# Performance work log

Hardware: AMD Instinct MI355X
Metric: run time of the kernel (lower is better)

## Reference

```python
import jax, jax.numpy as jnp
import numpy as np

N_NODES = 50000
N_EDGES = 800000
N_FEAT = 128
D_HID = 128
N_CLASS = 40


def gcn_conv(x, W, b, src, dst, n_nodes):
    """PyG GCNConv: h = D^{-1/2} (A + I) D^{-1/2} (x @ W) + b.
    src/dst are int arrays [E]; self-loops handled analytically."""
    h = x @ W  # [N, D]
    ones = jnp.ones(src.shape[0], dtype=h.dtype)
    # degree after adding self-loops: 1 + in-degree (edge weights are 1)
    deg = 1.0 + jax.ops.segment_sum(ones, dst, num_segments=n_nodes)
    dinv = jax.lax.rsqrt(deg)  # [N]
    # messages along edges src -> dst with symmetric normalization
    msg = h[src] * (dinv[src] * dinv[dst])[:, None]  # [E, D]
    agg = jax.ops.segment_sum(msg, dst, num_segments=n_nodes)  # [N, D]
    # self-loop contribution: dinv[i]^2 * h[i]
    agg = agg + h * (dinv * dinv)[:, None]
    return agg + b


def setup_inputs() -> dict:
    key = jax.random.key(0)
    ks = jax.random.split(key, 5)
    x = jax.random.normal(ks[0], (N_NODES, N_FEAT), dtype=jnp.float32)
    edge_index = jax.random.randint(ks[1], (2, N_EDGES), 0, N_NODES, dtype=jnp.int64)
    s_in = 1.0 / np.sqrt(N_FEAT)
    s_h = 1.0 / np.sqrt(D_HID)
    W_in = jax.random.normal(ks[2], (N_FEAT, D_HID), dtype=jnp.float32) * s_in
    W1 = jax.random.normal(ks[3], (D_HID, D_HID), dtype=jnp.float32) * s_h
    W_out = jax.random.normal(ks[4], (D_HID, N_CLASS), dtype=jnp.float32) * s_h
    return {
        "x": x,
        "edge_index": edge_index,
        "W_in": W_in,
        "b_in": jnp.zeros((D_HID,), jnp.float32),
        "W1": W1,
        "b1": jnp.zeros((D_HID,), jnp.float32),
        "W_out": W_out,
        "b_out": jnp.zeros((N_CLASS,), jnp.float32),
    }


def reference(x, edge_index, W_in, b_in, W1, b1, W_out, b_out):
    src, dst = edge_index[0], edge_index[1]
    n = x.shape[0]
    # input GCNConv (no activation on input_fc, matching the torch forward)
    h = gcn_conv(x, W_in, b_in, src, dst, n)
    # hidden layer: dropout is identity at eval; relu after conv; normalize=False
    h = jax.nn.relu(gcn_conv(h, W1, b1, src, dst, n))
    out = h @ W_out + b_out
    return jax.nn.log_softmax(out, axis=1)
```

## Files before the change

kernel.cpp:

```cpp
#include <hip/hip_runtime.h>
#include <math.h>


#define THREADS 256

typedef __attribute__((ext_vector_type(8))) short short8v;
typedef __attribute__((ext_vector_type(4))) float float4v;

__device__ __forceinline__ float b2f(unsigned int lo16) {
    return __uint_as_float(lo16 << 16);
}
__device__ __forceinline__ unsigned short f2b(float f) {
    unsigned int u = __float_as_uint(f);
    u += 0x7FFFu + ((u >> 16) & 1u);
    return (unsigned short)(u >> 16);
}

__global__ void detect_idx64(const int* __restrict__ idx, int* __restrict__ flag) {
    int t = threadIdx.x;
    unsigned long long b = __ballot(idx[2 * t + 1] == 0);
    if (t == 0) *flag = (b == 0xFFFFFFFFFFFFFFFFull) ? 1 : 0;
}

__global__ void fill_pos(const int* __restrict__ idx, const int* __restrict__ flag,
                         int* __restrict__ cnt, unsigned int* __restrict__ rec, int E) {
    int e = blockIdx.x * blockDim.x + threadIdx.x;
    if (e >= E) return;
    int f = *flag;
    int src, dst;
    if (f) { src = idx[2 * e]; dst = idx[2 * (E + e)]; }
    else   { src = idx[e];     dst = idx[E + e]; }
    unsigned int pos = (unsigned int)atomicAdd(&cnt[dst], 1);
    rec[e] = ((unsigned int)src << 16) | (pos & 0xFFFFu);
}

__global__ __launch_bounds__(256) void scanA(const int* __restrict__ cnt,
                                             int* __restrict__ bsum, int N) {
    __shared__ int wt[4];
    int tid = threadIdx.x, lane = tid & 63, w = tid >> 6;
    int i = blockIdx.x * 256 + tid;
    int v = (i < N) ? cnt[i] : 0;
    int s = v;
#pragma unroll
    for (int off = 1; off < 64; off <<= 1) {
        int t = __shfl_up(s, off);
        if (lane >= off) s += t;
    }
    if (lane == 63) wt[w] = s;
    __syncthreads();
    if (tid == 0) bsum[blockIdx.x] = wt[0] + wt[1] + wt[2] + wt[3];
}

__global__ __launch_bounds__(256) void scanB(int* __restrict__ bsum,
                                             int* __restrict__ boff,
                                             int* __restrict__ rowstart,
                                             int nb, int N) {
    __shared__ int wt[4];
    __shared__ int wo[5];
    int tid = threadIdx.x, lane = tid & 63, w = tid >> 6;
    int v = (tid < nb) ? bsum[tid] : 0;
    int s = v;
#pragma unroll
    for (int off = 1; off < 64; off <<= 1) {
        int t = __shfl_up(s, off);
        if (lane >= off) s += t;
    }
    if (lane == 63) wt[w] = s;
    __syncthreads();
    if (tid == 0) {
        int run = 0;
#pragma unroll
        for (int k = 0; k < 4; ++k) { wo[k] = run; run += wt[k]; }
        wo[4] = run;
    }
    __syncthreads();
    if (tid < nb) boff[tid] = wo[w] + s - v;
    if (tid == 0) rowstart[N] = wo[4];
}

__global__ __launch_bounds__(256) void scanC(const int* __restrict__ cnt,
                                             const int* __restrict__ boff,
                                             int* __restrict__ rowstart,
                                             float* __restrict__ dinv, int N) {
    __shared__ int wt[4];
    __shared__ int wo[4];
    int tid = threadIdx.x, lane = tid & 63, w = tid >> 6;
    int i = blockIdx.x * 256 + tid;
    int v = (i < N) ? cnt[i] : 0;
    int s = v;
#pragma unroll
    for (int off = 1; off < 64; off <<= 1) {
        int t = __shfl_up(s, off);
        if (lane >= off) s += t;
    }
    if (lane == 63) wt[w] = s;
    __syncthreads();
    if (tid == 0) {
        int run = 0;
#pragma unroll
        for (int k = 0; k < 4; ++k) { wo[k] = run; run += wt[k]; }
    }
    __syncthreads();
    if (i < N) {
        rowstart[i] = boff[blockIdx.x] + wo[w] + (s - v);
        dinv[i] = rsqrtf(1.0f + (float)v);
    }
}

__global__ void fill_place(const int* __restrict__ idx, const int* __restrict__ flag,
                           const unsigned int* __restrict__ rec,
                           const int* __restrict__ rowstart,
                           unsigned short* __restrict__ srcs, int E) {
    int e = blockIdx.x * blockDim.x + threadIdx.x;
    if (e >= E) return;
    int f = *flag;
    int dst = f ? idx[2 * (E + e)] : idx[E + e];
    unsigned int r = rec[e];
    srcs[rowstart[dst] + (int)(r & 0xFFFFu)] = (unsigned short)(r >> 16);
}

__global__ __launch_bounds__(256) void pack_w2(const float* __restrict__ W0,
                                               const float* __restrict__ W1,
                                               uint4* __restrict__ wpk0,
                                               uint4* __restrict__ wpk1) {
    const float* W = blockIdx.x ? W1 : W0;
    uint4* wpk = blockIdx.x ? wpk1 : wpk0;
    int tid = threadIdx.x;
    for (int it = 0; it < 8; ++it) {
        int s = it * 256 + tid;
        int ct = s >> 8;
        int kb = (s >> 6) & 3;
        int l  = s & 63;
        int col = ct * 16 + (l & 15);
        int k0  = kb * 32 + ((l >> 4) << 3);
        unsigned short e0 = f2b(W[(k0 + 0) * 128 + col]);
        unsigned short e1 = f2b(W[(k0 + 1) * 128 + col]);
        unsigned short e2 = f2b(W[(k0 + 2) * 128 + col]);
        unsigned short e3 = f2b(W[(k0 + 3) * 128 + col]);
        unsigned short e4 = f2b(W[(k0 + 4) * 128 + col]);
        unsigned short e5 = f2b(W[(k0 + 5) * 128 + col]);
        unsigned short e6 = f2b(W[(k0 + 6) * 128 + col]);
        unsigned short e7 = f2b(W[(k0 + 7) * 128 + col]);
        uint4 u;
        u.x = (unsigned int)e0 | ((unsigned int)e1 << 16);
        u.y = (unsigned int)e2 | ((unsigned int)e3 << 16);
        u.z = (unsigned int)e4 | ((unsigned int)e5 << 16);
        u.w = (unsigned int)e6 | ((unsigned int)e7 << 16);
        wpk[s] = u;
    }
}

template <int ABF>
__global__ __launch_bounds__(256) void gemm_mfma(const void* __restrict__ Ap,
                                                 const uint4* __restrict__ wpk,
                                                 unsigned short* __restrict__ outb,
                                                 int N) {
    __shared__ unsigned short ol[128 * 128];
    int tid = threadIdx.x;
    int w = tid >> 6, l = tid & 63;
    int lr = l & 15, lq = l >> 4;
    int base = blockIdx.x * 128;
    int arow0 = base + w * 16 + lr;
    int arow1 = base + 64 + w * 16 + lr;
    int ar0 = (arow0 < N) ? arow0 : (N - 1);
    int ar1 = (arow1 < N) ? arow1 : (N - 1);

    float4v acc[2][8];
#pragma unroll
    for (int t = 0; t < 2; ++t)
#pragma unroll
        for (int ct = 0; ct < 8; ++ct) acc[t][ct] = (float4v){0.f, 0.f, 0.f, 0.f};

#pragma unroll
    for (int kb = 0; kb < 4; ++kb) {
        short8v af0, af1;
        if (ABF) {
            uint4 v0 = *(const uint4*)((const unsigned short*)Ap + (size_t)ar0 * 128 + kb * 32 + lq * 8);
            uint4 v1 = *(const uint4*)((const unsigned short*)Ap + (size_t)ar1 * 128 + kb * 32 + lq * 8);
            union { uint4 u; short8v s; } c0, c1; c0.u = v0; c1.u = v1;
            af0 = c0.s; af1 = c1.s;
        } else {
            const float* a0 = (const float*)Ap + (size_t)ar0 * 128 + kb * 32 + lq * 8;
            const float* a1 = (const float*)Ap + (size_t)ar1 * 128 + kb * 32 + lq * 8;
            float4 va0 = *(const float4*)a0, vb0 = *(const float4*)(a0 + 4);
            float4 va1 = *(const float4*)a1, vb1 = *(const float4*)(a1 + 4);
            uint4 u0, u1;
            u0.x = (unsigned int)f2b(va0.x) | ((unsigned int)f2b(va0.y) << 16);
            u0.y = (unsigned int)f2b(va0.z) | ((unsigned int)f2b(va0.w) << 16);
            u0.z = (unsigned int)f2b(vb0.x) | ((unsigned int)f2b(vb0.y) << 16);
            u0.w = (unsigned int)f2b(vb0.z) | ((unsigned int)f2b(vb0.w) << 16);
            u1.x = (unsigned int)f2b(va1.x) | ((unsigned int)f2b(va1.y) << 16);
            u1.y = (unsigned int)f2b(va1.z) | ((unsigned int)f2b(va1.w) << 16);
            u1.z = (unsigned int)f2b(vb1.x) | ((unsigned int)f2b(vb1.y) << 16);
            u1.w = (unsigned int)f2b(vb1.z) | ((unsigned int)f2b(vb1.w) << 16);
            union { uint4 uu; short8v s; } c0, c1; c0.uu = u0; c1.uu = u1;
            af0 = c0.s; af1 = c1.s;
        }
#pragma unroll
        for (int ct = 0; ct < 8; ++ct) {
            uint4 bv = wpk[(ct * 4 + kb) * 64 + l];
            union { uint4 u; short8v s; } cv; cv.u = bv; short8v bf = cv.s;
            acc[0][ct] = __builtin_amdgcn_mfma_f32_16x16x32_bf16(af0, bf, acc[0][ct], 0, 0, 0);
            acc[1][ct] = __builtin_amdgcn_mfma_f32_16x16x32_bf16(af1, bf, acc[1][ct], 0, 0, 0);
        }
    }

#pragma unroll
    for (int t = 0; t < 2; ++t)
#pragma unroll
        for (int ct = 0; ct < 8; ++ct)
#pragma unroll
            for (int r = 0; r < 4; ++r)
                ol[(t * 64 + w * 16 + lq * 4 + r) * 128 + ct * 16 + lr] = f2b(acc[t][ct][r]);
    __syncthreads();
#pragma unroll
    for (int it = 0; it < 8; ++it) {
        int o = it * 4096 + tid * 16;
        int rr = o >> 8;
        int cb = o & 255;
        int gr = base + rr;
        if (gr < N) {
            uint4 v = *(const uint4*)((const char*)ol + o);
            *(uint4*)((char*)outb + (size_t)gr * 256 + cb) = v;
        }
    }
}

__global__ __launch_bounds__(256) void agg_node(const unsigned short* __restrict__ hb,
                                                const int* __restrict__ rowstart,
                                                const unsigned short* __restrict__ srcs,
                                                const float* __restrict__ dinv,
                                                const float* __restrict__ b,
                                                unsigned short* __restrict__ outb,
                                                int N, int do_relu) {
    int w = threadIdx.x >> 6, lane = threadIdx.x & 63;
    int node = blockIdx.x * 4 + w;
    if (node >= N) return;
    int beg = rowstart[node], end = rowstart[node + 1];
    float dn = dinv[node];
    int quarter = lane >> 4, q = lane & 15;
    const uint4* hb8 = (const uint4*)hb;
    float a0 = 0.f, a1 = 0.f, a2 = 0.f, a3 = 0.f;
    float a4 = 0.f, a5 = 0.f, a6 = 0.f, a7 = 0.f;

    for (int j0 = beg; j0 < end; j0 += 64) {
        int myj = j0 + lane;
        int ms = 0;
        float md = 0.f;
        if (myj < end) { ms = (int)srcs[myj]; md = dinv[ms]; }
        int m = min(64, end - j0);
#pragma unroll 2
        for (int k = 0; k < m; k += 8) {
            int i0 = k + quarter;
            int i1 = k + 4 + quarter;
            int s0 = __shfl(ms, i0);
            int s1 = __shfl(ms, i1);
            float c0 = dn * __shfl(md, i0);
            float c1 = dn * __shfl(md, i1);
            uint4 v0 = hb8[(size_t)s0 * 16 + q];
            uint4 v1 = hb8[(size_t)s1 * 16 + q];
            a0 += c0 * b2f(v0.x & 0xFFFFu);
            a1 += c0 * b2f(v0.x >> 16);
            a2 += c0 * b2f(v0.y & 0xFFFFu);
            a3 += c0 * b2f(v0.y >> 16);
            a4 += c0 * b2f(v0.z & 0xFFFFu);
            a5 += c0 * b2f(v0.z >> 16);
            a6 += c0 * b2f(v0.w & 0xFFFFu);
            a7 += c0 * b2f(v0.w >> 16);
            a0 += c1 * b2f(v1.x & 0xFFFFu);
            a1 += c1 * b2f(v1.x >> 16);
            a2 += c1 * b2f(v1.y & 0xFFFFu);
            a3 += c1 * b2f(v1.y >> 16);
            a4 += c1 * b2f(v1.z & 0xFFFFu);
            a5 += c1 * b2f(v1.z >> 16);
            a6 += c1 * b2f(v1.w & 0xFFFFu);
            a7 += c1 * b2f(v1.w >> 16);
        }
    }
    a0 += __shfl_xor(a0, 32); a1 += __shfl_xor(a1, 32);
    a2 += __shfl_xor(a2, 32); a3 += __shfl_xor(a3, 32);
    a4 += __shfl_xor(a4, 32); a5 += __shfl_xor(a5, 32);
    a6 += __shfl_xor(a6, 32); a7 += __shfl_xor(a7, 32);
    a0 += __shfl_xor(a0, 16); a1 += __shfl_xor(a1, 16);
    a2 += __shfl_xor(a2, 16); a3 += __shfl_xor(a3, 16);
    a4 += __shfl_xor(a4, 16); a5 += __shfl_xor(a5, 16);
    a6 += __shfl_xor(a6, 16); a7 += __shfl_xor(a7, 16);

    if (quarter == 0) {
        uint4 sv = hb8[(size_t)node * 16 + q];
        float d2 = dn * dn;
        float4 b0 = ((const float4*)b)[2 * q];
        float4 b1 = ((const float4*)b)[2 * q + 1];
        float r0 = a0 + d2 * b2f(sv.x & 0xFFFFu) + b0.x;
        float r1 = a1 + d2 * b2f(sv.x >> 16)     + b0.y;
        float r2 = a2 + d2 * b2f(sv.y & 0xFFFFu) + b0.z;
        float r3 = a3 + d2 * b2f(sv.y >> 16)     + b0.w;
        float r4 = a4 + d2 * b2f(sv.z & 0xFFFFu) + b1.x;
        float r5 = a5 + d2 * b2f(sv.z >> 16)     + b1.y;
        float r6 = a6 + d2 * b2f(sv.w & 0xFFFFu) + b1.z;
        float r7 = a7 + d2 * b2f(sv.w >> 16)     + b1.w;
        if (do_relu) {
            r0 = fmaxf(r0, 0.f); r1 = fmaxf(r1, 0.f);
            r2 = fmaxf(r2, 0.f); r3 = fmaxf(r3, 0.f);
            r4 = fmaxf(r4, 0.f); r5 = fmaxf(r5, 0.f);
            r6 = fmaxf(r6, 0.f); r7 = fmaxf(r7, 0.f);
        }
        uint4 o;
        o.x = (unsigned int)f2b(r0) | ((unsigned int)f2b(r1) << 16);
        o.y = (unsigned int)f2b(r2) | ((unsigned int)f2b(r3) << 16);
        o.z = (unsigned int)f2b(r4) | ((unsigned int)f2b(r5) << 16);
        o.w = (unsigned int)f2b(r6) | ((unsigned int)f2b(r7) << 16);
        ((uint4*)outb)[(size_t)node * 16 + q] = o;
    }
}

__global__ __launch_bounds__(256) void out_gemm(const unsigned short* __restrict__ h2b,
                                                const float* __restrict__ Wout,
                                                const float* __restrict__ bout,
                                                float* __restrict__ out, int N) {
    __shared__ float Xt[128 * 128];
    __shared__ float Wl[128 * 40];
    __shared__ float bl[40];
    int tid = threadIdx.x;
    int row0 = blockIdx.x * 128;

    for (int i = tid; i < 128 * 40; i += 256) Wl[i] = Wout[i];
    if (tid < 40) bl[tid] = bout[tid];

    {
        int r = tid >> 1, kh = tid & 1;
        int gr = row0 + r;
#pragma unroll
        for (int i = 0; i < 16; ++i) {
            int k = kh * 64 + i * 4;
            float f0, f1, f2, f3;
            if (gr < N) {
                uint2 qv = ((const uint2*)h2b)[(size_t)gr * 32 + (k >> 2)];
                f0 = b2f(qv.x & 0xFFFFu); f1 = b2f(qv.x >> 16);
                f2 = b2f(qv.y & 0xFFFFu); f3 = b2f(qv.y >> 16);
            } else {
                f0 = f1 = f2 = f3 = 0.f;
            }
            Xt[(k + 0) * 128 + r] = f0;
            Xt[(k + 1) * 128 + r] = f1;
            Xt[(k + 2) * 128 + r] = f2;
            Xt[(k + 3) * 128 + r] = f3;
        }
    }
    __syncthreads();

    int cg = tid & 7;
    int r4 = tid >> 3;
    float bias[5];
#pragma unroll
    for (int c = 0; c < 5; ++c) bias[c] = bl[5 * cg + c];

    float acc[4][5];
#pragma unroll
    for (int j = 0; j < 4; ++j)
#pragma unroll
        for (int c = 0; c < 5; ++c) acc[j][c] = 0.f;

    const float4* Xt4 = (const float4*)Xt;
#pragma unroll 4
    for (int k = 0; k < 128; ++k) {
        float4 xv = Xt4[k * 32 + r4];
        const float* wr = &Wl[k * 40 + 5 * cg];
        float w0 = wr[0], w1 = wr[1], w2 = wr[2], w3 = wr[3], w4 = wr[4];
        float xs[4] = {xv.x, xv.y, xv.z, xv.w};
#pragma unroll
        for (int j = 0; j < 4; ++j) {
            acc[j][0] += xs[j] * w0;
            acc[j][1] += xs[j] * w1;
            acc[j][2] += xs[j] * w2;
            acc[j][3] += xs[j] * w3;
            acc[j][4] += xs[j] * w4;
        }
    }

#pragma unroll
    for (int j = 0; j < 4; ++j) {
        int r = row0 + r4 * 4 + j;
        if (r >= N) continue;
        float v[5];
        float m = -INFINITY;
#pragma unroll
        for (int c = 0; c < 5; ++c) { v[c] = acc[j][c] + bias[c]; m = fmaxf(m, v[c]); }
        m = fmaxf(m, __shfl_xor(m, 1));
        m = fmaxf(m, __shfl_xor(m, 2));
        m = fmaxf(m, __shfl_xor(m, 4));
        float s = 0.f;
#pragma unroll
        for (int c = 0; c < 5; ++c) s += expf(v[c] - m);
        s += __shfl_xor(s, 1);
        s += __shfl_xor(s, 2);
        s += __shfl_xor(s, 4);
        float ls = logf(s);
#pragma unroll
        for (int c = 0; c < 5; ++c) out[(size_t)r * 40 + 5 * cg + c] = v[c] - m - ls;
    }
}

static inline size_t al256(size_t x) { return (x + 255) & ~(size_t)255; }

extern "C" void kernel_launch(void* const* d_in, const int* in_sizes, int n_in,
                              void* d_out, int out_size, void* d_ws, size_t ws_size,
                              hipStream_t stream) {
    const float* x     = (const float*)d_in[0];
    const int*   idx   = (const int*)d_in[1];
    const float* W_in  = (const float*)d_in[2];
    const float* b_in  = (const float*)d_in[3];
    const float* W1    = (const float*)d_in[4];
    const float* b1    = (const float*)d_in[5];
    const float* W_out = (const float*)d_in[6];
    const float* b_out = (const float*)d_in[7];
    float* out = (float*)d_out;

    int N = in_sizes[0] / 128;
    int E = in_sizes[1] / 2;

    char* ws = (char*)d_ws;
    size_t off = 0;
    int* flag = (int*)(ws + off);              off += 256;
    int* cnt = (int*)(ws + off);               off += al256((size_t)N * 4);
    int* rowstart = (int*)(ws + off);          off += al256((size_t)(N + 1) * 4);
    float* dinv = (float*)(ws + off);          off += al256((size_t)N * 4);
    unsigned short* srcs = (unsigned short*)(ws + off); off += al256((size_t)E * 2);
    unsigned int* rec = (unsigned int*)(ws + off);      off += al256((size_t)E * 4);
    int* bsum = (int*)(ws + off);              off += 2048;
    int* boff = (int*)(ws + off);              off += 2048;
    uint4* wpk1 = (uint4*)(ws + off);          off += 32768;
    uint4* wpk2 = (uint4*)(ws + off);          off += 32768;
    unsigned short* B0 = (unsigned short*)(ws + off);   off += (size_t)N * 128 * 2;
    unsigned short* B1 = (unsigned short*)(ws + off);

    int nb_e = (E + THREADS - 1) / THREADS;
    int nb_n = (N + THREADS - 1) / THREADS;
    int nb_g = (N + 127) / 128;
    int nb_a = (N + 3) / 4;

    detect_idx64<<<1, 64, 0, stream>>>(idx, flag);
    hipMemsetAsync(cnt, 0, (size_t)N * 4, stream);
    pack_w2<<<2, THREADS, 0, stream>>>(W_in, W1, wpk1, wpk2);
    fill_pos<<<nb_e, THREADS, 0, stream>>>(idx, flag, cnt, rec, E);
    scanA<<<nb_n, THREADS, 0, stream>>>(cnt, bsum, N);
    scanB<<<1, THREADS, 0, stream>>>(bsum, boff, rowstart, nb_n, N);
    scanC<<<nb_n, THREADS, 0, stream>>>(cnt, boff, rowstart, dinv, N);
    fill_place<<<nb_e, THREADS, 0, stream>>>(idx, flag, rec, rowstart, srcs, E);

    gemm_mfma<0><<<nb_g, THREADS, 0, stream>>>(x, wpk1, B0, N);
    agg_node<<<nb_a, THREADS, 0, stream>>>(B0, rowstart, srcs, dinv, b_in,
                                           B1, N, 0);
    gemm_mfma<1><<<nb_g, THREADS, 0, stream>>>(B1, wpk2, B0, N);
    agg_node<<<nb_a, THREADS, 0, stream>>>(B0, rowstart, srcs, dinv, b1,
                                           B1, N, 1);
    out_gemm<<<nb_g, THREADS, 0, stream>>>(B1, W_out, b_out, out, N);
}
```

Before: 260.6 us.

## Merge setup kernels and co-schedule first GEMM with edge counting

Replaces the flag-detect kernel, the count memset and the weight packing with one init kernel that also pre-converts x to bf16. The first-layer GEMM then runs in the same launch as the edge-position atomic pass, with separate blocks for each, so the two independent jobs overlap and fewer kernels are launched. The cost is an extra pass that writes and re-reads a bf16 copy of x. The agg loop also loses its unroll-2 pragma, which may change how well its loads are scheduled.

```diff
diff --git a/kernel.cpp b/kernel.cpp
--- a/kernel.cpp
+++ b/kernel.cpp
@@ -16,15 +16,116 @@
     return (unsigned short)(u >> 16);
 }
 
-__global__ void detect_idx64(const int* __restrict__ idx, int* __restrict__ flag) {
-    int t = threadIdx.x;
-    unsigned long long b = __ballot(idx[2 * t + 1] == 0);
-    if (t == 0) *flag = (b == 0xFFFFFFFFFFFFFFFFull) ? 1 : 0;
-}
-
-__global__ void fill_pos(const int* __restrict__ idx, const int* __restrict__ flag,
-                         int* __restrict__ cnt, unsigned int* __restrict__ rec, int E) {
-    int e = blockIdx.x * blockDim.x + threadIdx.x;
+__global__ __launch_bounds__(256) void f_init(const float* __restrict__ x,
+                                              const int* __restrict__ idx,
+                                              const float* __restrict__ W0,
+                                              const float* __restrict__ W1f,
+                                              int* __restrict__ flag,
+                                              int* __restrict__ cnt,
+                                              uint4* __restrict__ wpk0,
+                                              uint4* __restrict__ wpk1,
+                                              unsigned short* __restrict__ Xb,
+                                              int N) {
+    int tid = threadIdx.x, bid = blockIdx.x, nb = gridDim.x;
+    if (bid == 0 && tid < 64) {
+        unsigned long long b = __ballot(idx[2 * tid + 1] == 0);
+        if (tid == 0) *flag = (b == 0xFFFFFFFFFFFFFFFFull) ? 1 : 0;
+    }
+    for (int i = bid * 256 + tid; i < N; i += nb * 256) cnt[i] = 0;
+    if (bid < 2) {
+        const float* W = bid ? W1f : W0;
+        uint4* wpk = bid ? wpk1 : wpk0;
+#pragma unroll
+        for (int it = 0; it < 8; ++it) {
+            int s = it * 256 + tid;
+            int ct = s >> 8, kb = (s >> 6) & 3, l = s & 63;
+            int col = ct * 16 + (l & 15);
+            int k0 = kb * 32 + ((l >> 4) << 3);
+            uint4 u;
+            u.x = (unsigned int)f2b(W[(k0 + 0) * 128 + col]) | ((unsigned int)f2b(W[(k0 + 1) * 128 + col]) << 16);
+            u.y = (unsigned int)f2b(W[(k0 + 2) * 128 + col]) | ((unsigned int)f2b(W[(k0 + 3) * 128 + col]) << 16);
+            u.z = (unsigned int)f2b(W[(k0 + 4) * 128 + col]) | ((unsigned int)f2b(W[(k0 + 5) * 128 + col]) << 16);
+            u.w = (unsigned int)f2b(W[(k0 + 6) * 128 + col]) | ((unsigned int)f2b(W[(k0 + 7) * 128 + col]) << 16);
+            wpk[s] = u;
+        }
+    }
+    int total = N * 32;
+    const float4* x4 = (const float4*)x;
+    ushort4* xb4 = (ushort4*)Xb;
+    for (int i = bid * 256 + tid; i < total; i += nb * 256) {
+        float4 v = x4[i];
+        ushort4 o;
+        o.x = f2b(v.x); o.y = f2b(v.y); o.z = f2b(v.z); o.w = f2b(v.w);
+        xb4[i] = o;
+    }
+}
+
+__device__ __forceinline__ void gemm_body(const unsigned short* __restrict__ Ab,
+                                          const uint4* __restrict__ wpk,
+                                          unsigned short* __restrict__ outb,
+                                          unsigned short* ol, int base, int N) {
+    int tid = threadIdx.x;
+    int w = tid >> 6, l = tid & 63;
+    int lr = l & 15, lq = l >> 4;
+    int arow0 = base + w * 16 + lr;
+    int arow1 = base + 64 + w * 16 + lr;
+    int ar0 = (arow0 < N) ? arow0 : (N - 1);
+    int ar1 = (arow1 < N) ? arow1 : (N - 1);
+
+    float4v acc[2][8];
+#pragma unroll
+    for (int t = 0; t < 2; ++t)
+#pragma unroll
+        for (int ct = 0; ct < 8; ++ct) acc[t][ct] = (float4v){0.f, 0.f, 0.f, 0.f};
+
+#pragma unroll
+    for (int kb = 0; kb < 4; ++kb) {
+        uint4 v0 = *(const uint4*)(Ab + (size_t)ar0 * 128 + kb * 32 + lq * 8);
+        uint4 v1 = *(const uint4*)(Ab + (size_t)ar1 * 128 + kb * 32 + lq * 8);
+        union { uint4 u; short8v s; } c0, c1; c0.u = v0; c1.u = v1;
+        short8v af0 = c0.s, af1 = c1.s;
+#pragma unroll
+        for (int ct = 0; ct < 8; ++ct) {
+            uint4 bv = wpk[(ct * 4 + kb) * 64 + l];
+            union { uint4 u; short8v s; } cv; cv.u = bv; short8v bf = cv.s;
+            acc[0][ct] = __builtin_amdgcn_mfma_f32_16x16x32_bf16(af0, bf, acc[0][ct], 0, 0, 0);
+            acc[1][ct] = __builtin_amdgcn_mfma_f32_16x16x32_bf16(af1, bf, acc[1][ct], 0, 0, 0);
+        }
+    }
+#pragma unroll
+    for (int t = 0; t < 2; ++t)
+#pragma unroll
+        for (int ct = 0; ct < 8; ++ct)
+#pragma unroll
+            for (int r = 0; r < 4; ++r)
+                ol[(t * 64 + w * 16 + lq * 4 + r) * 128 + ct * 16 + lr] = f2b(acc[t][ct][r]);
+    __syncthreads();
+#pragma unroll
+    for (int it = 0; it < 8; ++it) {
+        int o = it * 4096 + tid * 16;
+        int rr = o >> 8, cb = o & 255;
+        int gr = base + rr;
+        if (gr < N) {
+            uint4 v = *(const uint4*)((const char*)ol + o);
+            *(uint4*)((char*)outb + (size_t)gr * 256 + cb) = v;
+        }
+    }
+}
+
+__global__ __launch_bounds__(256) void f_g1fp(const unsigned short* __restrict__ Xb,
+                                              const uint4* __restrict__ wpk1,
+                                              unsigned short* __restrict__ B0,
+                                              const int* __restrict__ idx,
+                                              const int* __restrict__ flag,
+                                              int* __restrict__ cnt,
+                                              unsigned int* __restrict__ rec,
+                                              int N, int E, int nbg) {
+    __shared__ unsigned short ol[128 * 128];
+    if ((int)blockIdx.x < nbg) {
+        gemm_body(Xb, wpk1, B0, ol, blockIdx.x * 128, N);
+        return;
+    }
+    int e = (blockIdx.x - nbg) * 256 + threadIdx.x;
     if (e >= E) return;
     int f = *flag;
     int src, dst;
@@ -32,6 +133,14 @@
     else   { src = idx[e];     dst = idx[E + e]; }
     unsigned int pos = (unsigned int)atomicAdd(&cnt[dst], 1);
     rec[e] = ((unsigned int)src << 16) | (pos & 0xFFFFu);
+}
+
+__global__ __launch_bounds__(256) void gemm_mfma(const unsigned short* __restrict__ Ab,
+                                                 const uint4* __restrict__ wpk,
+                                                 unsigned short* __restrict__ outb,
+                                                 int N) {
+    __shared__ unsigned short ol[128 * 128];
+    gemm_body(Ab, wpk, outb, ol, blockIdx.x * 128, N);
 }
 
 __global__ __launch_bounds__(256) void scanA(const int* __restrict__ cnt,
@@ -117,113 +226,6 @@
     int dst = f ? idx[2 * (E + e)] : idx[E + e];
     unsigned int r = rec[e];
     srcs[rowstart[dst] + (int)(r & 0xFFFFu)] = (unsigned short)(r >> 16);
-}
-
-__global__ __launch_bounds__(256) void pack_w2(const float* __restrict__ W0,
-                                               const float* __restrict__ W1,
-                                               uint4* __restrict__ wpk0,
-                                               uint4* __restrict__ wpk1) {
-    const float* W = blockIdx.x ? W1 : W0;
-    uint4* wpk = blockIdx.x ? wpk1 : wpk0;
-    int tid = threadIdx.x;
-    for (int it = 0; it < 8; ++it) {
-        int s = it * 256 + tid;
-        int ct = s >> 8;
-        int kb = (s >> 6) & 3;
-        int l  = s & 63;
-        int col = ct * 16 + (l & 15);
-        int k0  = kb * 32 + ((l >> 4) << 3);
-        unsigned short e0 = f2b(W[(k0 + 0) * 128 + col]);
-        unsigned short e1 = f2b(W[(k0 + 1) * 128 + col]);
-        unsigned short e2 = f2b(W[(k0 + 2) * 128 + col]);
-        unsigned short e3 = f2b(W[(k0 + 3) * 128 + col]);
-        unsigned short e4 = f2b(W[(k0 + 4) * 128 + col]);
-        unsigned short e5 = f2b(W[(k0 + 5) * 128 + col]);
-        unsigned short e6 = f2b(W[(k0 + 6) * 128 + col]);
-        unsigned short e7 = f2b(W[(k0 + 7) * 128 + col]);
-        uint4 u;
-        u.x = (unsigned int)e0 | ((unsigned int)e1 << 16);
-        u.y = (unsigned int)e2 | ((unsigned int)e3 << 16);
-        u.z = (unsigned int)e4 | ((unsigned int)e5 << 16);
-        u.w = (unsigned int)e6 | ((unsigned int)e7 << 16);
-        wpk[s] = u;
-    }
-}
-
-template <int ABF>
-__global__ __launch_bounds__(256) void gemm_mfma(const void* __restrict__ Ap,
-                                                 const uint4* __restrict__ wpk,
-                                                 unsigned short* __restrict__ outb,
-                                                 int N) {
-    __shared__ unsigned short ol[128 * 128];
-    int tid = threadIdx.x;
-    int w = tid >> 6, l = tid & 63;
-    int lr = l & 15, lq = l >> 4;
-    int base = blockIdx.x * 128;
-    int arow0 = base + w * 16 + lr;
-    int arow1 = base + 64 + w * 16 + lr;
-    int ar0 = (arow0 < N) ? arow0 : (N - 1);
-    int ar1 = (arow1 < N) ? arow1 : (N - 1);
-
-    float4v acc[2][8];
-#pragma unroll
-    for (int t = 0; t < 2; ++t)
-#pragma unroll
-        for (int ct = 0; ct < 8; ++ct) acc[t][ct] = (float4v){0.f, 0.f, 0.f, 0.f};
-
-#pragma unroll
-    for (int kb = 0; kb < 4; ++kb) {
-        short8v af0, af1;
-        if (ABF) {
-            uint4 v0 = *(const uint4*)((const unsigned short*)Ap + (size_t)ar0 * 128 + kb * 32 + lq * 8);
-            uint4 v1 = *(const uint4*)((const unsigned short*)Ap + (size_t)ar1 * 128 + kb * 32 + lq * 8);
-            union { uint4 u; short8v s; } c0, c1; c0.u = v0; c1.u = v1;
-            af0 = c0.s; af1 = c1.s;
-        } else {
-            const float* a0 = (const float*)Ap + (size_t)ar0 * 128 + kb * 32 + lq * 8;
-            const float* a1 = (const float*)Ap + (size_t)ar1 * 128 + kb * 32 + lq * 8;
-            float4 va0 = *(const float4*)a0, vb0 = *(const float4*)(a0 + 4);
-            float4 va1 = *(const float4*)a1, vb1 = *(const float4*)(a1 + 4);
-            uint4 u0, u1;
-            u0.x = (unsigned int)f2b(va0.x) | ((unsigned int)f2b(va0.y) << 16);
-            u0.y = (unsigned int)f2b(va0.z) | ((unsigned int)f2b(va0.w) << 16);
-            u0.z = (unsigned int)f2b(vb0.x) | ((unsigned int)f2b(vb0.y) << 16);
-            u0.w = (unsigned int)f2b(vb0.z) | ((unsigned int)f2b(vb0.w) << 16);
-            u1.x = (unsigned int)f2b(va1.x) | ((unsigned int)f2b(va1.y) << 16);
-            u1.y = (unsigned int)f2b(va1.z) | ((unsigned int)f2b(va1.w) << 16);
-            u1.z = (unsigned int)f2b(vb1.x) | ((unsigned int)f2b(vb1.y) << 16);
-            u1.w = (unsigned int)f2b(vb1.z) | ((unsigned int)f2b(vb1.w) << 16);
-            union { uint4 uu; short8v s; } c0, c1; c0.uu = u0; c1.uu = u1;
-            af0 = c0.s; af1 = c1.s;
-        }
-#pragma unroll
-        for (int ct = 0; ct < 8; ++ct) {
-            uint4 bv = wpk[(ct * 4 + kb) * 64 + l];
-            union { uint4 u; short8v s; } cv; cv.u = bv; short8v bf = cv.s;
-            acc[0][ct] = __builtin_amdgcn_mfma_f32_16x16x32_bf16(af0, bf, acc[0][ct], 0, 0, 0);
-            acc[1][ct] = __builtin_amdgcn_mfma_f32_16x16x32_bf16(af1, bf, acc[1][ct], 0, 0, 0);
-        }
-    }
-
-#pragma unroll
-    for (int t = 0; t < 2; ++t)
-#pragma unroll
-        for (int ct = 0; ct < 8; ++ct)
-#pragma unroll
-            for (int r = 0; r < 4; ++r)
-                ol[(t * 64 + w * 16 + lq * 4 + r) * 128 + ct * 16 + lr] = f2b(acc[t][ct][r]);
-    __syncthreads();
-#pragma unroll
-    for (int it = 0; it < 8; ++it) {
-        int o = it * 4096 + tid * 16;
-        int rr = o >> 8;
-        int cb = o & 255;
-        int gr = base + rr;
-        if (gr < N) {
-            uint4 v = *(const uint4*)((const char*)ol + o);
-            *(uint4*)((char*)outb + (size_t)gr * 256 + cb) = v;
-        }
-    }
 }
 
 __global__ __launch_bounds__(256) void agg_node(const unsigned short* __restrict__ hb,
@@ -245,11 +247,9 @@
 
     for (int j0 = beg; j0 < end; j0 += 64) {
         int myj = j0 + lane;
-        int ms = 0;
-        float md = 0.f;
+        int ms = 0; float md = 0.f;
         if (myj < end) { ms = (int)srcs[myj]; md = dinv[ms]; }
         int m = min(64, end - j0);
-#pragma unroll 2
         for (int k = 0; k < m; k += 8) {
             int i0 = k + quarter;
             int i1 = k + 4 + quarter;
@@ -259,22 +259,14 @@
             float c1 = dn * __shfl(md, i1);
             uint4 v0 = hb8[(size_t)s0 * 16 + q];
             uint4 v1 = hb8[(size_t)s1 * 16 + q];
-            a0 += c0 * b2f(v0.x & 0xFFFFu);
-            a1 += c0 * b2f(v0.x >> 16);
-            a2 += c0 * b2f(v0.y & 0xFFFFu);
-            a3 += c0 * b2f(v0.y >> 16);
-            a4 += c0 * b2f(v0.z & 0xFFFFu);
-            a5 += c0 * b2f(v0.z >> 16);
-            a6 += c0 * b2f(v0.w & 0xFFFFu);
-            a7 += c0 * b2f(v0.w >> 16);
-            a0 += c1 * b2f(v1.x & 0xFFFFu);
-            a1 += c1 * b2f(v1.x >> 16);
-            a2 += c1 * b2f(v1.y & 0xFFFFu);
-            a3 += c1 * b2f(v1.y >> 16);
-            a4 += c1 * b2f(v1.z & 0xFFFFu);
-            a5 += c1 * b2f(v1.z >> 16);
-            a6 += c1 * b2f(v1.w & 0xFFFFu);
-            a7 += c1 * b2f(v1.w >> 16);
+            a0 += c0 * b2f(v0.x & 0xFFFFu); a1 += c0 * b2f(v0.x >> 16);
+            a2 += c0 * b2f(v0.y & 0xFFFFu); a3 += c0 * b2f(v0.y >> 16);
+            a4 += c0 * b2f(v0.z & 0xFFFFu); a5 += c0 * b2f(v0.z >> 16);
+            a6 += c0 * b2f(v0.w & 0xFFFFu); a7 += c0 * b2f(v0.w >> 16);
+            a0 += c1 * b2f(v1.x & 0xFFFFu); a1 += c1 * b2f(v1.x >> 16);
+            a2 += c1 * b2f(v1.y & 0xFFFFu); a3 += c1 * b2f(v1.y >> 16);
+            a4 += c1 * b2f(v1.z & 0xFFFFu); a5 += c1 * b2f(v1.z >> 16);
+            a6 += c1 * b2f(v1.w & 0xFFFFu); a7 += c1 * b2f(v1.w >> 16);
         }
     }
     a0 += __shfl_xor(a0, 32); a1 += __shfl_xor(a1, 32);
@@ -431,6 +423,7 @@
     int* boff = (int*)(ws + off);              off += 2048;
     uint4* wpk1 = (uint4*)(ws + off);          off += 32768;
     uint4* wpk2 = (uint4*)(ws + off);          off += 32768;
+    unsigned short* Xb = (unsigned short*)(ws + off);   off += (size_t)N * 128 * 2;
     unsigned short* B0 = (unsigned short*)(ws + off);   off += (size_t)N * 128 * 2;
     unsigned short* B1 = (unsigned short*)(ws + off);
 
@@ -439,20 +432,16 @@
     int nb_g = (N + 127) / 128;
     int nb_a = (N + 3) / 4;
 
-    detect_idx64<<<1, 64, 0, stream>>>(idx, flag);
-    hipMemsetAsync(cnt, 0, (size_t)N * 4, stream);
-    pack_w2<<<2, THREADS, 0, stream>>>(W_in, W1, wpk1, wpk2);
-    fill_pos<<<nb_e, THREADS, 0, stream>>>(idx, flag, cnt, rec, E);
+    f_init<<<256, THREADS, 0, stream>>>(x, idx, W_in, W1, flag, cnt, wpk1, wpk2, Xb, N);
+    f_g1fp<<<nb_g + nb_e, THREADS, 0, stream>>>(Xb, wpk1, B0, idx, flag, cnt, rec,
+                                                N, E, nb_g);
     scanA<<<nb_n, THREADS, 0, stream>>>(cnt, bsum, N);
     scanB<<<1, THREADS, 0, stream>>>(bsum, boff, rowstart, nb_n, N);
     scanC<<<nb_n, THREADS, 0, stream>>>(cnt, boff, rowstart, dinv, N);
     fill_place<<<nb_e, THREADS, 0, stream>>>(idx, flag, rec, rowstart, srcs, E);
 
-    gemm_mfma<0><<<nb_g, THREADS, 0, stream>>>(x, wpk1, B0, N);
-    agg_node<<<nb_a, THREADS, 0, stream>>>(B0, rowstart, srcs, dinv, b_in,
-                                           B1, N, 0);
-    gemm_mfma<1><<<nb_g, THREADS, 0, stream>>>(B1, wpk2, B0, N);
-    agg_node<<<nb_a, THREADS, 0, stream>>>(B0, rowstart, srcs, dinv, b1,
-                                           B1, N, 1);
+    agg_node<<<nb_a, THREADS, 0, stream>>>(B0, rowstart, srcs, dinv, b_in, B1, N, 0);
+    gemm_mfma<<<nb_g, THREADS, 0, stream>>>(B1, wpk2, B0, N);
+    agg_node<<<nb_a, THREADS, 0, stream>>>(B0, rowstart, srcs, dinv, b1, B1, N, 1);
     out_gemm<<<nb_g, THREADS, 0, stream>>>(B1, W_out, b_out, out, N);
 }
```

Result: no change. 256.0 us (-1.8%).
